# Performance work log

Hardware: AMD Instinct MI355X
Metric: run time of the kernel (lower is better)

The kernel has to match this reference:

```python
import jax, jax.numpy as jnp
import numpy as np

N_NODES = 100000
N_EDGES = 3200000
IN_FEATS = 128
OUT_FEATS = 64


def setup_inputs() -> dict:
    key = jax.random.key(0)
    k1, k2, k3, k4 = jax.random.split(key, 4)
    features = jax.random.normal(k1, (N_NODES, IN_FEATS), dtype=jnp.float32)
    W = jax.random.normal(k2, (IN_FEATS, OUT_FEATS), dtype=jnp.float32) * (1.0 / np.sqrt(IN_FEATS))
    b = jnp.zeros((OUT_FEATS,), dtype=jnp.float32)
    src = jax.random.randint(k3, (N_EDGES,), 0, N_NODES, dtype=jnp.int32)
    dst = jax.random.randint(k4, (N_EDGES,), 0, N_NODES, dtype=jnp.int32)
    return {"features": features, "W": W, "b": b, "src": src, "dst": dst}


def reference(features, W, b, src, dst):
    # DGL GraphConv with norm='both':
    #   h = D_dst^{-1/2} * (A^T @ (D_src^{-1/2} * X @ W)) + b
    # (W applied before aggregation since in_feats > out_feats, as DGL does)
    N = features.shape[0]
    ones = jnp.ones(src.shape[0], dtype=features.dtype)
    out_deg = jax.ops.segment_sum(ones, src, num_segments=N)
    in_deg = jax.ops.segment_sum(ones, dst, num_segments=N)
    out_norm = jax.lax.rsqrt(jnp.clip(out_deg, 1.0))  # [N]
    in_norm = jax.lax.rsqrt(jnp.clip(in_deg, 1.0))    # [N]
    x = (features * out_norm[:, None]) @ W            # [N, out_feats]
    msgs = x[src]                                     # [E, out_feats] irregular gather
    agg = jax.ops.segment_sum(msgs, dst, num_segments=N)  # [N, out_feats] scatter-add
    h = agg * in_norm[:, None] + b                    # [N, out_feats]
    return h.mean(axis=1)                             # [N], mean over feature dim
```

## Files before the change

### kernel.cpp

```cpp
#include <hip/hip_runtime.h>

#define NN 100000
#define NE 3200000
#define IN_F 128
#define OUT_F 64

#define BW_SHIFT 9
#define BWIDTH 512
#define NB 196
#define CAP 20480
#define CB 256
#define EPB (NE / CB)
#define NQ (EPB / 4)

__global__ __launch_bounds__(1024) void bin_kernel(const int* __restrict__ src,
                                                   const int* __restrict__ dst,
                                                   int* __restrict__ curS_g,
                                                   int* __restrict__ curD_g,
                                                   unsigned short* __restrict__ srcloc,
                                                   int* __restrict__ pack,
                                                   const float* __restrict__ W,
                                                   const float* __restrict__ bias,
                                                   float* __restrict__ wbar,
                                                   float* __restrict__ bbar) {
    __shared__ int hs[NB];
    __shared__ int hd[NB];
    __shared__ int cS[NB];
    __shared__ int cD[NB];
    const int blk = blockIdx.x;
    const int t = threadIdx.x;
    for (int k = t; k < NB; k += 1024) { hs[k] = 0; hd[k] = 0; }
    __syncthreads();

    const int4* s4 = (const int4*)(src + blk * EPB);
    const int4* d4 = (const int4*)(dst + blk * EPB);
    int4 sc[4], dc[4];
    #pragma unroll
    for (int u = 0; u < 4; ++u) {
        int i = t + u * 1024;
        if (i < NQ) { sc[u] = s4[i]; dc[u] = d4[i]; }
        else        { sc[u] = make_int4(-1, -1, -1, -1); dc[u] = sc[u]; }
    }
    #pragma unroll
    for (int u = 0; u < 4; ++u) {
        if (sc[u].x >= 0) {
            atomicAdd(&hs[sc[u].x >> BW_SHIFT], 1);
            atomicAdd(&hs[sc[u].y >> BW_SHIFT], 1);
            atomicAdd(&hs[sc[u].z >> BW_SHIFT], 1);
            atomicAdd(&hs[sc[u].w >> BW_SHIFT], 1);
            atomicAdd(&hd[dc[u].x >> BW_SHIFT], 1);
            atomicAdd(&hd[dc[u].y >> BW_SHIFT], 1);
            atomicAdd(&hd[dc[u].z >> BW_SHIFT], 1);
            atomicAdd(&hd[dc[u].w >> BW_SHIFT], 1);
        }
    }
    __syncthreads();
    for (int k = t; k < NB; k += 1024) {
        cS[k] = k * CAP + atomicAdd(&curS_g[k], hs[k]);
        cD[k] = k * CAP + atomicAdd(&curD_g[k], hd[k]);
    }
    __syncthreads();
    #pragma unroll
    for (int u = 0; u < 4; ++u) {
        if (sc[u].x >= 0) {
            int p;
            p = atomicAdd(&cS[sc[u].x >> BW_SHIFT], 1); srcloc[p] = (unsigned short)(sc[u].x & (BWIDTH - 1));
            p = atomicAdd(&cS[sc[u].y >> BW_SHIFT], 1); srcloc[p] = (unsigned short)(sc[u].y & (BWIDTH - 1));
            p = atomicAdd(&cS[sc[u].z >> BW_SHIFT], 1); srcloc[p] = (unsigned short)(sc[u].z & (BWIDTH - 1));
            p = atomicAdd(&cS[sc[u].w >> BW_SHIFT], 1); srcloc[p] = (unsigned short)(sc[u].w & (BWIDTH - 1));
            p = atomicAdd(&cD[dc[u].x >> BW_SHIFT], 1); pack[p] = sc[u].x | ((dc[u].x & (BWIDTH - 1)) << 17);
            p = atomicAdd(&cD[dc[u].y >> BW_SHIFT], 1); pack[p] = sc[u].y | ((dc[u].y & (BWIDTH - 1)) << 17);
            p = atomicAdd(&cD[dc[u].z >> BW_SHIFT], 1); pack[p] = sc[u].z | ((dc[u].z & (BWIDTH - 1)) << 17);
            p = atomicAdd(&cD[dc[u].w >> BW_SHIFT], 1); pack[p] = sc[u].w | ((dc[u].w & (BWIDTH - 1)) << 17);
        }
    }
    if (blk == 0) {
        if (t < IN_F) {
            float s = 0.f;
            for (int j = 0; j < OUT_F; ++j) s += W[t * OUT_F + j];
            wbar[t] = s * (1.0f / OUT_F);
        } else if (t == IN_F) {
            float sb = 0.f;
            for (int j = 0; j < OUT_F; ++j) sb += bias[j];
            *bbar = sb * (1.0f / OUT_F);
        }
    }
}

__global__ __launch_bounds__(1024) void bucket_scalar_kernel(const unsigned short* __restrict__ srcloc,
                                                             const int* __restrict__ curS_g,
                                                             const float* __restrict__ features,
                                                             const float* __restrict__ wbar,
                                                             float* __restrict__ sval) {
    __shared__ int cnt[BWIDTH];
    __shared__ float wsh[IN_F];
    const int k = blockIdx.x;
    const int t = threadIdx.x;
    if (t < IN_F) wsh[t] = wbar[t];
    for (int i = t; i < BWIDTH; i += 1024) cnt[i] = 0;
    __syncthreads();
    const int base = k * CAP;
    const int len = curS_g[k];
    for (int i = t; i < len; i += 1024) atomicAdd(&cnt[srcloc[base + i]], 1);
    __syncthreads();
    const int lane = t & 63;
    const int wave = t >> 6;
    const float2 w = ((const float2*)wsh)[lane];
    for (int j = 0; j < 32; ++j) {
        const int loc = wave * 32 + j;
        const int node = (k << BW_SHIFT) + loc;
        if (node >= NN) break;
        float2 f = ((const float2*)(features + (size_t)node * IN_F))[lane];
        float p = f.x * w.x + f.y * w.y;
        #pragma unroll
        for (int off = 32; off > 0; off >>= 1) p += __shfl_down(p, off);
        if (lane == 0) sval[node] = p * rsqrtf(fmaxf((float)cnt[loc], 1.0f));
    }
}

__global__ __launch_bounds__(1024) void accum_kernel(const int* __restrict__ pack,
                                                     const int* __restrict__ curD_g,
                                                     const float* __restrict__ sval,
                                                     const float* __restrict__ bbar,
                                                     float* __restrict__ out) {
    __shared__ float agg[BWIDTH];
    __shared__ int cnt[BWIDTH];
    const int k = blockIdx.x;
    const int t = threadIdx.x;
    for (int i = t; i < BWIDTH; i += 1024) { agg[i] = 0.f; cnt[i] = 0; }
    __syncthreads();
    const int base = k * CAP;
    const int len = curD_g[k];
    for (int i = t; i < len; i += 1024) {
        int p = pack[base + i];
        int s = p & 0x1FFFF;
        int loc = (p >> 17) & (BWIDTH - 1);
        float v = sval[s];
        atomicAdd(&agg[loc], v);
        atomicAdd(&cnt[loc], 1);
    }
    __syncthreads();
    for (int i = t; i < BWIDTH; i += 1024) {
        int node = (k << BW_SHIFT) + i;
        if (node < NN) out[node] = agg[i] * rsqrtf(fmaxf((float)cnt[i], 1.0f)) + bbar[0];
    }
}

__global__ void wbar_fb_kernel(const float* __restrict__ W, const float* __restrict__ bias,
                               float* __restrict__ wbar, float* __restrict__ bbar) {
    int k = threadIdx.x;
    float s = 0.f;
    for (int j = 0; j < OUT_F; ++j) s += W[k * OUT_F + j];
    wbar[k] = s * (1.0f / OUT_F);
    if (k == 0) {
        float sb = 0.f;
        for (int j = 0; j < OUT_F; ++j) sb += bias[j];
        *bbar = sb * (1.0f / OUT_F);
    }
}
__global__ void deg_kernel(const int* __restrict__ src, const int* __restrict__ dst,
                           int* __restrict__ deg_out, int* __restrict__ deg_in) {
    const int nq = NE / 4;
    int i = blockIdx.x * blockDim.x + threadIdx.x;
    const int stride = gridDim.x * blockDim.x;
    const int4* src4 = (const int4*)src;
    const int4* dst4 = (const int4*)dst;
    for (; i < nq; i += stride) {
        int4 s = src4[i];
        int4 d = dst4[i];
        atomicAdd(&deg_out[s.x], 1); atomicAdd(&deg_out[s.y], 1);
        atomicAdd(&deg_out[s.z], 1); atomicAdd(&deg_out[s.w], 1);
        atomicAdd(&deg_in[d.x], 1);  atomicAdd(&deg_in[d.y], 1);
        atomicAdd(&deg_in[d.z], 1);  atomicAdd(&deg_in[d.w], 1);
    }
}
__global__ void node_scalar_deg_kernel(const float* __restrict__ features,
                                       const int* __restrict__ deg_out,
                                       const float* __restrict__ wbar,
                                       float* __restrict__ sval) {
    const int lane = threadIdx.x & 63;
    const int wave = threadIdx.x >> 6;
    const int node = blockIdx.x * 4 + wave;
    if (node >= NN) return;
    const float2* f2 = (const float2*)(features + (size_t)node * IN_F);
    const float2* w2 = (const float2*)wbar;
    float2 f = f2[lane];
    float2 w = w2[lane];
    float p = f.x * w.x + f.y * w.y;
    #pragma unroll
    for (int off = 32; off > 0; off >>= 1) p += __shfl_down(p, off);
    if (lane == 0) {
        float d = (float)deg_out[node];
        sval[node] = p * rsqrtf(fmaxf(d, 1.0f));
    }
}
__global__ void scatter_kernel(const int* __restrict__ src, const int* __restrict__ dst,
                               const float* __restrict__ sval, float* __restrict__ agg) {
    const int nq = NE / 4;
    int i = blockIdx.x * blockDim.x + threadIdx.x;
    const int stride = gridDim.x * blockDim.x;
    const int4* src4 = (const int4*)src;
    const int4* dst4 = (const int4*)dst;
    for (; i < nq; i += stride) {
        int4 s = src4[i];
        int4 d = dst4[i];
        atomicAdd(&agg[d.x], sval[s.x]);
        atomicAdd(&agg[d.y], sval[s.y]);
        atomicAdd(&agg[d.z], sval[s.z]);
        atomicAdd(&agg[d.w], sval[s.w]);
    }
}
__global__ void final_kernel(const float* __restrict__ agg, const int* __restrict__ deg_in,
                             const float* __restrict__ bbar, float* __restrict__ out) {
    int n = blockIdx.x * blockDim.x + threadIdx.x;
    if (n >= NN) return;
    float d = (float)deg_in[n];
    out[n] = agg[n] * rsqrtf(fmaxf(d, 1.0f)) + *bbar;
}

extern "C" void kernel_launch(void* const* d_in, const int* in_sizes, int n_in,
                              void* d_out, int out_size, void* d_ws, size_t ws_size,
                              hipStream_t stream) {
    const float* features = (const float*)d_in[0];
    const float* W        = (const float*)d_in[1];
    const float* bias     = (const float*)d_in[2];
    const int*   src      = (const int*)d_in[3];
    const int*   dst      = (const int*)d_in[4];
    float* out = (float*)d_out;

    size_t need_words = (size_t)NB * CAP + (size_t)NB * CAP / 2 + 2 * NB
                      + (size_t)NN + IN_F + 1;
    if (ws_size >= need_words * 4 + 64) {
        int* w_ = (int*)d_ws;
        int*  pack              = w_;
        unsigned short* srcloc  = (unsigned short*)(w_ + (size_t)NB * CAP);
        int*  curS_g            = w_ + (size_t)NB * CAP + (size_t)NB * CAP / 2;
        int*  curD_g            = curS_g + NB;
        float* sval             = (float*)(curD_g + NB);
        float* wbar             = sval + NN;
        float* bbar             = wbar + IN_F;

        hipMemsetAsync(curS_g, 0, 2 * NB * sizeof(int), stream);
        bin_kernel<<<CB, 1024, 0, stream>>>(src, dst, curS_g, curD_g, srcloc, pack,
                                            W, bias, wbar, bbar);
        bucket_scalar_kernel<<<NB, 1024, 0, stream>>>(srcloc, curS_g, features, wbar, sval);
        accum_kernel<<<NB, 1024, 0, stream>>>(pack, curD_g, sval, bbar, out);
    } else {
        int*   deg_out = (int*)d_ws;
        int*   deg_in  = deg_out + NN;
        float* agg     = (float*)(deg_in + NN);
        float* sval    = agg + NN;
        float* wbar    = sval + NN;
        float* bbar    = wbar + IN_F;
        hipMemsetAsync(d_ws, 0, (size_t)3 * NN * sizeof(int), stream);
        wbar_fb_kernel<<<1, 128, 0, stream>>>(W, bias, wbar, bbar);
        deg_kernel<<<2048, 256, 0, stream>>>(src, dst, deg_out, deg_in);
        node_scalar_deg_kernel<<<(NN + 3) / 4, 256, 0, stream>>>(features, deg_out, wbar, sval);
        scatter_kernel<<<2048, 256, 0, stream>>>(src, dst, sval, agg);
        final_kernel<<<(NN + 255) / 256, 256, 0, stream>>>(agg, deg_in, bbar, out);
    }
}
```

Before: 189.7 us.

## Stage binned edges in shared memory and vectorize per-node feature dot products

The binning kernel now computes a local exclusive scan of per-bucket counts, scatters edges into shared-memory staging buffers, then copies each bucket's contiguous run to global memory with coalesced wave-wide writes, replacing scattered per-edge global stores. The bucket scalar kernel processes four nodes per wave with float4 loads and a 16-lane xor reduction instead of one node per wave with float2 loads. The staging uses about 75KB of shared memory per 1024-thread block and adds several barriers for the scans, which may limit occupancy.

```diff
diff --git a/kernel.cpp b/kernel.cpp
--- a/kernel.cpp
+++ b/kernel.cpp
@@ -23,10 +23,13 @@
                                                    const float* __restrict__ bias,
                                                    float* __restrict__ wbar,
                                                    float* __restrict__ bbar) {
-    __shared__ int hs[NB];
-    __shared__ int hd[NB];
-    __shared__ int cS[NB];
-    __shared__ int cD[NB];
+    __shared__ int hs[NB], hd[NB];
+    __shared__ int lS[NB], lD[NB];
+    __shared__ int cS[NB], cD[NB];
+    __shared__ int gS[NB], gD[NB];
+    __shared__ int scanbuf[256];
+    __shared__ unsigned short stS[EPB];
+    __shared__ int stD[EPB];
     const int blk = blockIdx.x;
     const int t = threadIdx.x;
     for (int k = t; k < NB; k += 1024) { hs[k] = 0; hd[k] = 0; }
@@ -55,24 +58,53 @@
         }
     }
     __syncthreads();
-    for (int k = t; k < NB; k += 1024) {
-        cS[k] = k * CAP + atomicAdd(&curS_g[k], hs[k]);
-        cD[k] = k * CAP + atomicAdd(&curD_g[k], hd[k]);
+    if (t < 256) scanbuf[t] = (t < NB) ? hs[t] : 0;
+    __syncthreads();
+    #pragma unroll
+    for (int off = 1; off < 256; off <<= 1) {
+        int x = (t < 256 && t >= off) ? scanbuf[t - off] : 0;
+        __syncthreads();
+        if (t < 256) scanbuf[t] += x;
+        __syncthreads();
+    }
+    if (t < NB) { int e = scanbuf[t] - hs[t]; lS[t] = e; cS[t] = e; }
+    __syncthreads();
+    if (t < 256) scanbuf[t] = (t < NB) ? hd[t] : 0;
+    __syncthreads();
+    #pragma unroll
+    for (int off = 1; off < 256; off <<= 1) {
+        int x = (t < 256 && t >= off) ? scanbuf[t - off] : 0;
+        __syncthreads();
+        if (t < 256) scanbuf[t] += x;
+        __syncthreads();
+    }
+    if (t < NB) { int e = scanbuf[t] - hd[t]; lD[t] = e; cD[t] = e; }
+    if (t < NB) {
+        gS[t] = t * CAP + atomicAdd(&curS_g[t], hs[t]);
+        gD[t] = t * CAP + atomicAdd(&curD_g[t], hd[t]);
     }
     __syncthreads();
     #pragma unroll
     for (int u = 0; u < 4; ++u) {
         if (sc[u].x >= 0) {
             int p;
-            p = atomicAdd(&cS[sc[u].x >> BW_SHIFT], 1); srcloc[p] = (unsigned short)(sc[u].x & (BWIDTH - 1));
-            p = atomicAdd(&cS[sc[u].y >> BW_SHIFT], 1); srcloc[p] = (unsigned short)(sc[u].y & (BWIDTH - 1));
-            p = atomicAdd(&cS[sc[u].z >> BW_SHIFT], 1); srcloc[p] = (unsigned short)(sc[u].z & (BWIDTH - 1));
-            p = atomicAdd(&cS[sc[u].w >> BW_SHIFT], 1); srcloc[p] = (unsigned short)(sc[u].w & (BWIDTH - 1));
-            p = atomicAdd(&cD[dc[u].x >> BW_SHIFT], 1); pack[p] = sc[u].x | ((dc[u].x & (BWIDTH - 1)) << 17);
-            p = atomicAdd(&cD[dc[u].y >> BW_SHIFT], 1); pack[p] = sc[u].y | ((dc[u].y & (BWIDTH - 1)) << 17);
-            p = atomicAdd(&cD[dc[u].z >> BW_SHIFT], 1); pack[p] = sc[u].z | ((dc[u].z & (BWIDTH - 1)) << 17);
-            p = atomicAdd(&cD[dc[u].w >> BW_SHIFT], 1); pack[p] = sc[u].w | ((dc[u].w & (BWIDTH - 1)) << 17);
-        }
+            p = atomicAdd(&cS[sc[u].x >> BW_SHIFT], 1); stS[p] = (unsigned short)(sc[u].x & (BWIDTH - 1));
+            p = atomicAdd(&cS[sc[u].y >> BW_SHIFT], 1); stS[p] = (unsigned short)(sc[u].y & (BWIDTH - 1));
+            p = atomicAdd(&cS[sc[u].z >> BW_SHIFT], 1); stS[p] = (unsigned short)(sc[u].z & (BWIDTH - 1));
+            p = atomicAdd(&cS[sc[u].w >> BW_SHIFT], 1); stS[p] = (unsigned short)(sc[u].w & (BWIDTH - 1));
+            p = atomicAdd(&cD[dc[u].x >> BW_SHIFT], 1); stD[p] = sc[u].x | ((dc[u].x & (BWIDTH - 1)) << 17);
+            p = atomicAdd(&cD[dc[u].y >> BW_SHIFT], 1); stD[p] = sc[u].y | ((dc[u].y & (BWIDTH - 1)) << 17);
+            p = atomicAdd(&cD[dc[u].z >> BW_SHIFT], 1); stD[p] = sc[u].z | ((dc[u].z & (BWIDTH - 1)) << 17);
+            p = atomicAdd(&cD[dc[u].w >> BW_SHIFT], 1); stD[p] = sc[u].w | ((dc[u].w & (BWIDTH - 1)) << 17);
+        }
+    }
+    __syncthreads();
+    const int wv = t >> 6, ln = t & 63;
+    for (int k = wv; k < NB; k += 16) {
+        int len = hs[k], lb = lS[k], gb = gS[k];
+        for (int j = ln; j < len; j += 64) srcloc[gb + j] = stS[lb + j];
+        len = hd[k]; lb = lD[k]; gb = gD[k];
+        for (int j = ln; j < len; j += 64) pack[gb + j] = stD[lb + j];
     }
     if (blk == 0) {
         if (t < IN_F) {
@@ -93,28 +125,32 @@
                                                              const float* __restrict__ wbar,
                                                              float* __restrict__ sval) {
     __shared__ int cnt[BWIDTH];
-    __shared__ float wsh[IN_F];
+    __shared__ float4 wsh[IN_F / 4];
     const int k = blockIdx.x;
     const int t = threadIdx.x;
-    if (t < IN_F) wsh[t] = wbar[t];
+    if (t < IN_F / 4) wsh[t] = ((const float4*)wbar)[t];
     for (int i = t; i < BWIDTH; i += 1024) cnt[i] = 0;
     __syncthreads();
     const int base = k * CAP;
     const int len = curS_g[k];
     for (int i = t; i < len; i += 1024) atomicAdd(&cnt[srcloc[base + i]], 1);
     __syncthreads();
-    const int lane = t & 63;
-    const int wave = t >> 6;
-    const float2 w = ((const float2*)wsh)[lane];
-    for (int j = 0; j < 32; ++j) {
-        const int loc = wave * 32 + j;
+    const int wv = t >> 6, ln = t & 63;
+    const int sub = ln >> 4, sl = ln & 15;
+    const float4 wa = wsh[sl], wb = wsh[sl + 16];
+    #pragma unroll
+    for (int it = 0; it < 8; ++it) {
+        const int loc = (wv << 5) + (it << 2) + sub;
         const int node = (k << BW_SHIFT) + loc;
-        if (node >= NN) break;
-        float2 f = ((const float2*)(features + (size_t)node * IN_F))[lane];
-        float p = f.x * w.x + f.y * w.y;
-        #pragma unroll
-        for (int off = 32; off > 0; off >>= 1) p += __shfl_down(p, off);
-        if (lane == 0) sval[node] = p * rsqrtf(fmaxf((float)cnt[loc], 1.0f));
+        if (node < NN) {
+            const float4* f4 = (const float4*)(features + (size_t)node * IN_F);
+            float4 fa = f4[sl], fb = f4[sl + 16];
+            float p = fa.x * wa.x + fa.y * wa.y + fa.z * wa.z + fa.w * wa.w
+                    + fb.x * wb.x + fb.y * wb.y + fb.z * wb.z + fb.w * wb.w;
+            #pragma unroll
+            for (int off = 1; off < 16; off <<= 1) p += __shfl_xor(p, off);
+            if (sl == 0) sval[node] = p * rsqrtf(fmaxf((float)cnt[loc], 1.0f));
+        }
     }
 }
 
```

After: 159.2 us. 1.19x faster.
